# Kernel tuning notes

Measured on AMD Instinct MI355X. Metric: run time of the kernel, lower is better.

## Reference

```python
import jax, jax.numpy as jnp
import numpy as np

VTH = 1.0  # config['v_threshold']
DT = 1.0


def spike_fn(x):
    # forward of ActFun_adp: heaviside(mem - vth)
    return (x > 0).astype(x.dtype)


def setup_inputs() -> dict:
    key = jax.random.key(0)
    k0, k1, k2, k3, k4 = jax.random.split(key, 5)
    B, T, D, H, O = 256, 250, 700, 1024, 20
    input_data = jax.random.normal(k0, (B, T, D), dtype=jnp.float32)
    # dense_1: nn.Linear(700, hidden) default init ~ U(-1/sqrt(D), 1/sqrt(D)); normal/sqrt(D) is an equivalent-scale stand-in
    W1 = jax.random.normal(k1, (H, D), dtype=jnp.float32) / np.sqrt(D).astype(np.float32)
    b1 = jnp.zeros((H,), dtype=jnp.float32)
    tau_m1 = jax.random.uniform(k2, (H,), dtype=jnp.float32, minval=0.0, maxval=4.0)
    # dense_2: xavier_normal_ weight, zero bias
    W2 = jax.random.normal(k3, (O, H), dtype=jnp.float32) * np.sqrt(2.0 / (H + O)).astype(np.float32)
    b2 = jnp.zeros((O,), dtype=jnp.float32)
    tau_m2 = jax.random.uniform(k4, (O,), dtype=jnp.float32, minval=0.0, maxval=4.0)
    return {"input_data": input_data, "W1": W1, "b1": b1, "tau_m1": tau_m1,
            "W2": W2, "b2": b2, "tau_m2": tau_m2}


def reference(input_data, W1, b1, tau_m1, W2, b2, tau_m2):
    B, T, D = input_data.shape
    H = W1.shape[0]
    O = W2.shape[0]
    alpha1 = jax.nn.sigmoid(tau_m1)  # [H]
    alpha2 = jax.nn.sigmoid(tau_m2)  # [O]
    # dense_1 is time-invariant: precompute projections for all timesteps [T,B,H]
    d1_all = (jnp.einsum('btd,hd->bth', input_data, W1) + b1).transpose(1, 0, 2)

    def step(carry, xs):
        mem1, spk1, mem2, acc = carry
        d1_t, i = xs
        # LIF layer 1: soft reset via -vth*spike (mem_update_pra, R_m=1, dt=1)
        mem1 = mem1 * alpha1 + (1.0 - alpha1) * d1_t - VTH * spk1 * DT
        spk1 = spike_fn(mem1 - VTH)
        # readout integrator
        d2 = spk1 @ W2.T + b2
        mem2 = mem2 * alpha2 + (1.0 - alpha2) * d2
        # accumulate softmax for i > 10
        gate = jnp.where(i > 10, jnp.float32(1.0), jnp.float32(0.0))
        acc = acc + gate * jax.nn.softmax(mem2, axis=1)
        return (mem1, spk1, mem2, acc), None

    init = (jnp.zeros((B, H), jnp.float32), jnp.zeros((B, H), jnp.float32),
            jnp.zeros((B, O), jnp.float32), jnp.zeros((B, O), jnp.float32))
    (_, _, _, acc), _ = jax.lax.scan(step, init, (d1_all, jnp.arange(T)))
    return acc
```

## Files before the change

### kernel.cpp

```cpp
#include <hip/hip_runtime.h>
#include <hip/hip_bf16.h>

#define B_  256
#define T_  250
#define D_  700
#define H_  1024
#define O_  20
#define KP  704
#define M_  64000
#define NT  22

typedef __attribute__((ext_vector_type(8))) short bf16x8;
typedef __attribute__((ext_vector_type(4))) float f32x4;

__device__ __forceinline__ void gl_lds16(const void* g, void* l) {
    __builtin_amdgcn_global_load_lds(
        (const __attribute__((address_space(1))) unsigned int*)g,
        (__attribute__((address_space(3))) unsigned int*)l, 16, 0, 0);
}

__global__ void split_convert(const float* __restrict__ src,
                              unsigned short* __restrict__ hi,
                              unsigned short* __restrict__ lo,
                              int M, int Kin, int Kout)
{
    int idx = blockIdx.x * blockDim.x + threadIdx.x;
    int chunks = Kout >> 3;
    int total = M * chunks;
    if (idx >= total) return;
    int m  = idx / chunks;
    int c  = idx - m * chunks;
    int d0 = c << 3;
    float x[8];
    if (d0 + 8 <= Kin) {
        const float4* p = (const float4*)(src + (long)m * Kin + d0);
        float4 v0 = p[0], v1 = p[1];
        x[0] = v0.x; x[1] = v0.y; x[2] = v0.z; x[3] = v0.w;
        x[4] = v1.x; x[5] = v1.y; x[6] = v1.z; x[7] = v1.w;
    } else {
#pragma unroll
        for (int e = 0; e < 8; ++e) {
            int d = d0 + e;
            x[e] = (d < Kin) ? src[(long)m * Kin + d] : 0.0f;
        }
    }
    unsigned short h8[8], l8[8];
#pragma unroll
    for (int e = 0; e < 8; ++e) {
        __hip_bfloat16 h = __float2bfloat16(x[e]);
        float hf = __bfloat162float(h);
        __hip_bfloat16 lv = __float2bfloat16(x[e] - hf);
        h8[e] = *(unsigned short*)&h;
        l8[e] = *(unsigned short*)&lv;
    }
    long ob = (long)m * Kout + d0;
    *(uint4*)(hi + ob) = *(uint4*)h8;
    *(uint4*)(lo + ob) = *(uint4*)l8;
}

#define MF(a,b,c) (c) = __builtin_amdgcn_mfma_f32_16x16x32_bf16((a),(b),(c),0,0,0)

__global__ __launch_bounds__(512, 2) void gemm256(
    const unsigned short* __restrict__ Ahi, const unsigned short* __restrict__ Alo,
    const unsigned short* __restrict__ Bhi, const unsigned short* __restrict__ Blo,
    const float* __restrict__ bias, float* __restrict__ C)
{
    __shared__ __align__(16) unsigned short sAh[2 * 8192];
    __shared__ __align__(16) unsigned short sAl[2 * 8192];
    __shared__ __align__(16) unsigned short sBh[2 * 8192];
    __shared__ __align__(16) unsigned short sBl[2 * 8192];

    const int bid = blockIdx.x;
    const int wg  = (bid & 7) * 125 + (bid >> 3);
    const int mblk = wg >> 2;
    const int nblk = wg & 3;

    const int t    = threadIdx.x;
    const int wave = t >> 6, lane = t & 63;
    const int wr = wave >> 2, wc = wave & 3;

    const int  ch0    = wave * 2;
    const int  rowoff = lane >> 2;
    const int  slotl  = (lane & 3) ^ ((lane >> 3) & 3);
    const long GCH    = 16L * KP;
    const long gArow  = (long)(mblk * 256 + rowoff) * KP + slotl * 8;
    const long gBrow  = (long)(nblk * 256 + rowoff) * KP + slotl * 8;
    const int  ldsl   = ch0 * 512 + lane * 8;

    const int fr   = lane & 15, fq = lane >> 4;
    const int fxor = ((fq ^ ((fr >> 1) & 3)) << 3);
    const int abase = (wr * 128 + fr) * 32 + fxor;
    const int bbase = (wc * 64 + fr) * 32 + fxor;

    f32x4 acc[8][4];
#pragma unroll
    for (int i = 0; i < 8; ++i)
#pragma unroll
        for (int j = 0; j < 4; ++j) acc[i][j] = (f32x4){0.f, 0.f, 0.f, 0.f};

    gl_lds16(Ahi + gArow + ch0 * GCH,       &sAh[ldsl]);
    gl_lds16(Ahi + gArow + (ch0 + 1) * GCH, &sAh[ldsl + 512]);
    gl_lds16(Bhi + gBrow + ch0 * GCH,       &sBh[ldsl]);
    gl_lds16(Bhi + gBrow + (ch0 + 1) * GCH, &sBh[ldsl + 512]);
    gl_lds16(Alo + gArow + ch0 * GCH,       &sAl[ldsl]);
    gl_lds16(Alo + gArow + (ch0 + 1) * GCH, &sAl[ldsl + 512]);
    gl_lds16(Blo + gBrow + ch0 * GCH,       &sBl[ldsl]);
    gl_lds16(Blo + gBrow + (ch0 + 1) * GCH, &sBl[ldsl + 512]);
    asm volatile("s_waitcnt vmcnt(0)" ::: "memory");
    __builtin_amdgcn_s_barrier();

    for (int tt = 0; tt < NT; ++tt) {
        const int  cur = (tt & 1) ? 8192 : 0;
        const int  nxt = 8192 - cur;
        const long ksn = (long)(tt + 1) * 32;
        const bool pf  = (tt + 1 < NT);

        bf16x8 bh[4], bl[4];
#pragma unroll
        for (int p = 0; p < 4; ++p) {
            const int i0 = 2 * p, i1 = 2 * p + 1;
            bf16x8 ah0 = *(const bf16x8*)&sAh[cur + abase + i0 * 512];
            bf16x8 ah1 = *(const bf16x8*)&sAh[cur + abase + i1 * 512];
            bf16x8 al0 = *(const bf16x8*)&sAl[cur + abase + i0 * 512];
            bf16x8 al1 = *(const bf16x8*)&sAl[cur + abase + i1 * 512];
            if (p == 0) {
#pragma unroll
                for (int j = 0; j < 4; ++j) {
                    bh[j] = *(const bf16x8*)&sBh[cur + bbase + j * 512];
                    bl[j] = *(const bf16x8*)&sBl[cur + bbase + j * 512];
                }
            }
            if (p == 0 && pf) {
                gl_lds16(Ahi + gArow + ch0 * GCH + ksn,       &sAh[nxt + ldsl]);
                gl_lds16(Ahi + gArow + (ch0 + 1) * GCH + ksn, &sAh[nxt + ldsl + 512]);
                gl_lds16(Bhi + gBrow + ch0 * GCH + ksn,       &sBh[nxt + ldsl]);
                gl_lds16(Bhi + gBrow + (ch0 + 1) * GCH + ksn, &sBh[nxt + ldsl + 512]);
            }
            if (p == 1 && pf) {
                gl_lds16(Alo + gArow + ch0 * GCH + ksn,       &sAl[nxt + ldsl]);
                gl_lds16(Alo + gArow + (ch0 + 1) * GCH + ksn, &sAl[nxt + ldsl + 512]);
                gl_lds16(Blo + gBrow + ch0 * GCH + ksn,       &sBl[nxt + ldsl]);
                gl_lds16(Blo + gBrow + (ch0 + 1) * GCH + ksn, &sBl[nxt + ldsl + 512]);
            }
            __builtin_amdgcn_s_barrier();
            asm volatile("s_waitcnt lgkmcnt(0)" ::: "memory");
            __builtin_amdgcn_sched_barrier(0);
            __builtin_amdgcn_s_setprio(1);
#pragma unroll
            for (int j = 0; j < 4; ++j) MF(ah0, bh[j], acc[i0][j]);
#pragma unroll
            for (int j = 0; j < 4; ++j) MF(ah1, bh[j], acc[i1][j]);
#pragma unroll
            for (int j = 0; j < 4; ++j) MF(ah0, bl[j], acc[i0][j]);
#pragma unroll
            for (int j = 0; j < 4; ++j) MF(ah1, bl[j], acc[i1][j]);
#pragma unroll
            for (int j = 0; j < 4; ++j) MF(al0, bh[j], acc[i0][j]);
#pragma unroll
            for (int j = 0; j < 4; ++j) MF(al1, bh[j], acc[i1][j]);
            __builtin_amdgcn_s_setprio(0);
            if (p == 3) asm volatile("s_waitcnt vmcnt(0)" ::: "memory");
            __builtin_amdgcn_s_barrier();
        }
    }

    const int r0 = mblk * 256 + wr * 128 + fq * 4;
    const int cc = nblk * 256 + wc * 64 + fr;
#pragma unroll
    for (int j = 0; j < 4; ++j) {
        int col = cc + j * 16;
        float bv = bias[col];
#pragma unroll
        for (int i = 0; i < 8; ++i) {
            int row = r0 + i * 16;
#pragma unroll
            for (int r = 0; r < 4; ++r)
                C[(long)(row + r) * H_ + col] = acc[i][j][r] + bv;
        }
    }
}

__global__ __launch_bounds__(256) void lif_spikes(
    const float* __restrict__ d1,
    const float* __restrict__ tau1,
    unsigned long long* __restrict__ spk)
{
    const int b    = blockIdx.y;
    const int h    = blockIdx.x * 256 + threadIdx.x;
    const int lane = threadIdx.x & 63;
    const int widx = blockIdx.x * 4 + (threadIdx.x >> 6);

    float tv  = tau1[h];
    float a1  = 1.0f / (1.0f + __expf(-tv));
    float om1 = 1.0f - a1;
    float mem = 0.f, sp = 0.f;

    const float* dp = d1 + (long)b * T_ * H_ + h;
    unsigned long long* op = spk + (long)b * T_ * 16 + widx;

    float p0 = dp[0],        p1 = dp[1L * H_], p2 = dp[2L * H_];
    float p3 = dp[3L * H_],  p4 = dp[4L * H_], p5 = dp[5L * H_];

    for (int ts = 0; ts < T_; ++ts) {
        float cur = p0;
        p0 = p1; p1 = p2; p2 = p3; p3 = p4; p4 = p5;
        int nts = ts + 6; nts = (nts < T_) ? nts : (T_ - 1);
        p5 = dp[(long)nts * H_];

        mem = mem * a1 + om1 * cur - sp;
        sp  = (mem > 1.0f) ? 1.0f : 0.0f;
        unsigned long long msk = __ballot(mem > 1.0f);
        if (lane == 0) op[(long)ts * 16] = msk;
    }
}

__global__ __launch_bounds__(256) void readout_dots(
    const unsigned long long* __restrict__ spk,
    const float* __restrict__ W2,
    float* __restrict__ d2t)
{
    const int t = threadIdx.x, wave = t >> 6, lane = t & 63;

    float w2r[5][16];
#pragma unroll
    for (int oo = 0; oo < 5; ++oo)
#pragma unroll
        for (int q = 0; q < 4; ++q)
            *(float4*)&w2r[oo][4 * q] =
                *(const float4*)&W2[(wave * 5 + oo) * H_ + lane * 16 + 4 * q];

    const int rbase = blockIdx.x * 32;
    int b0 = rbase / T_;
    int ts0 = rbase - b0 * T_;

    for (int i = 0; i < 32; i += 2) {
        int r0 = rbase + i, r1 = r0 + 1;
        unsigned long long bw0 = spk[(long)r0 * 16 + (lane >> 2)];
        unsigned long long bw1 = spk[(long)r1 * 16 + (lane >> 2)];
        unsigned int bits0 = (unsigned int)(bw0 >> ((lane & 3) * 16)) & 0xFFFFu;
        unsigned int bits1 = (unsigned int)(bw1 >> ((lane & 3) * 16)) & 0xFFFFu;
        float pa0[5] = {0, 0, 0, 0, 0}, pa1[5] = {0, 0, 0, 0, 0};
#pragma unroll
        for (int j = 0; j < 16; ++j) {
            float f0 = (bits0 >> j) & 1u ? 1.0f : 0.0f;
            float f1 = (bits1 >> j) & 1u ? 1.0f : 0.0f;
#pragma unroll
            for (int oo = 0; oo < 5; ++oo) {
                pa0[oo] = fmaf(f0, w2r[oo][j], pa0[oo]);
                pa1[oo] = fmaf(f1, w2r[oo][j], pa1[oo]);
            }
        }
#pragma unroll
        for (int m = 1; m < 64; m <<= 1)
#pragma unroll
            for (int oo = 0; oo < 5; ++oo) {
                pa0[oo] += __shfl_xor(pa0[oo], m, 64);
                pa1[oo] += __shfl_xor(pa1[oo], m, 64);
            }
        if (lane == 0) {
            int bA = b0, tsA = ts0 + i;
            if (tsA >= T_) { tsA -= T_; bA += 1; }
            int bB = bA, tsB = tsA + 1;
            if (tsB >= T_) { tsB = 0; bB += 1; }
#pragma unroll
            for (int oo = 0; oo < 5; ++oo) {
                d2t[(long)(wave * 5 + oo) * M_ + tsA * 256 + bA] = pa0[oo];
                d2t[(long)(wave * 5 + oo) * M_ + tsB * 256 + bB] = pa1[oo];
            }
        }
    }
}

__global__ __launch_bounds__(64) void mem2_scan(
    const float* __restrict__ d2t,
    const float* __restrict__ tau2, const float* __restrict__ b2,
    float* __restrict__ m2t)
{
    const int o = blockIdx.x;
    const int b = blockIdx.y * 64 + threadIdx.x;
    float tv  = tau2[o];
    float a2  = 1.0f / (1.0f + __expf(-tv));
    float om2 = 1.0f - a2;
    float bv  = b2[o];

    const float* dp = d2t + (long)o * M_ + b;
    float*       mp = m2t + (long)o * M_ + b;
    float mem = 0.f;

    float p0 = dp[0], p1 = dp[256], p2 = dp[512], p3 = dp[768];
    for (int ts = 0; ts < T_; ++ts) {
        float cur = p0; p0 = p1; p1 = p2; p2 = p3;
        int nts = ts + 4; nts = (nts < T_) ? nts : (T_ - 1);
        p3 = dp[(long)nts * 256];
        mem = mem * a2 + om2 * (cur + bv);
        mp[(long)ts * 256] = mem;
    }
}

__global__ __launch_bounds__(256) void softmax_acc(
    const float* __restrict__ m2t,
    float* __restrict__ out)
{
    __shared__ float sp[T_][O_];
    const int b  = blockIdx.x;
    const int ts = threadIdx.x;

    if (ts < T_) {
        if (ts > 10) {
            float m[O_];
#pragma unroll
            for (int o = 0; o < O_; ++o)
                m[o] = m2t[(long)o * M_ + ts * 256 + b];
            float mx = m[0];
#pragma unroll
            for (int o = 1; o < O_; ++o) mx = fmaxf(mx, m[o]);
            float s = 0.f;
#pragma unroll
            for (int o = 0; o < O_; ++o) { m[o] = __expf(m[o] - mx); s += m[o]; }
            float inv = 1.0f / s;
#pragma unroll
            for (int o = 0; o < O_; ++o) sp[ts][o] = m[o] * inv;
        } else {
#pragma unroll
            for (int o = 0; o < O_; ++o) sp[ts][o] = 0.f;
        }
    }
    __syncthreads();
    if (ts < O_) {
        float s = 0.f;
        for (int k = 11; k < T_; ++k) s += sp[k][ts];
        out[b * O_ + ts] = s;
    }
}

extern "C" void kernel_launch(void* const* d_in, const int* in_sizes, int n_in,
                              void* d_out, int out_size, void* d_ws, size_t ws_size,
                              hipStream_t stream)
{
    const float* X    = (const float*)d_in[0];
    const float* W1   = (const float*)d_in[1];
    const float* b1   = (const float*)d_in[2];
    const float* tau1 = (const float*)d_in[3];
    const float* W2   = (const float*)d_in[4];
    const float* b2   = (const float*)d_in[5];
    const float* tau2 = (const float*)d_in[6];
    float* out = (float*)d_out;

    unsigned short* Xhi  = (unsigned short*)d_ws;
    unsigned short* Xlo  = Xhi + (long)M_ * KP;
    unsigned short* W1hi = Xlo + (long)M_ * KP;
    unsigned short* W1lo = W1hi + (long)H_ * KP;
    float* d1 = (float*)(W1lo + (long)H_ * KP);

    unsigned long long* spk = (unsigned long long*)Xhi;
    float* d2t = (float*)Xlo;
    float* m2t = d2t + (long)O_ * M_;

    {
        int chunks = M_ * (KP / 8);
        split_convert<<<(chunks + 255) / 256, 256, 0, stream>>>(X, Xhi, Xlo, M_, D_, KP);
    }
    {
        int chunks = H_ * (KP / 8);
        split_convert<<<(chunks + 255) / 256, 256, 0, stream>>>(W1, W1hi, W1lo, H_, D_, KP);
    }

    gemm256<<<dim3(1000), dim3(512), 0, stream>>>(Xhi, Xlo, W1hi, W1lo, b1, d1);

    {
        dim3 grid(H_ / 256, B_);
        lif_spikes<<<grid, 256, 0, stream>>>(d1, tau1, spk);
    }

    readout_dots<<<M_ / 32, 256, 0, stream>>>(spk, W2, d2t);

    {
        dim3 grid(O_, 4);
        mem2_scan<<<grid, 64, 0, stream>>>(d2t, tau2, b2, m2t);
    }

    softmax_acc<<<B_, 256, 0, stream>>>(m2t, out);
}
```

Baseline: 795.6 us.

## Split GEMM tile loads into staged chunks with partial vmcnt waits and fewer barriers

Reworks the double-buffered K loop of the bf16 split-precision GEMM. Each wave now loads A rows in two groups (rows 0-3 and 4-7 chunks) plus the B chunks, and waits with partial vmcnt counts instead of draining all loads at the end of every K step. This lets compute on the first half of A start while the second half is still arriving. Barriers drop from two per phase to two per K step. The cost is correctness that now depends on a precise vmcnt ordering and on the chunk-to-wave mapping matching the LDS read pattern, which adds risk of races.

```diff
diff --git a/kernel.cpp b/kernel.cpp
--- a/kernel.cpp
+++ b/kernel.cpp
@@ -60,6 +60,28 @@
 
 #define MF(a,b,c) (c) = __builtin_amdgcn_mfma_f32_16x16x32_bf16((a),(b),(c),0,0,0)
 
+__device__ __forceinline__ void phase_mfma(
+    const bf16x8 ah0, const bf16x8 ah1, const bf16x8 al0, const bf16x8 al1,
+    const bf16x8* bh, const bf16x8* bl, f32x4* acc0, f32x4* acc1)
+{
+    asm volatile("s_waitcnt lgkmcnt(0)" ::: "memory");
+    __builtin_amdgcn_sched_barrier(0);
+    __builtin_amdgcn_s_setprio(1);
+#pragma unroll
+    for (int j = 0; j < 4; ++j) MF(ah0, bh[j], acc0[j]);
+#pragma unroll
+    for (int j = 0; j < 4; ++j) MF(ah1, bh[j], acc1[j]);
+#pragma unroll
+    for (int j = 0; j < 4; ++j) MF(ah0, bl[j], acc0[j]);
+#pragma unroll
+    for (int j = 0; j < 4; ++j) MF(ah1, bl[j], acc1[j]);
+#pragma unroll
+    for (int j = 0; j < 4; ++j) MF(al0, bh[j], acc0[j]);
+#pragma unroll
+    for (int j = 0; j < 4; ++j) MF(al1, bh[j], acc1[j]);
+    __builtin_amdgcn_s_setprio(0);
+}
+
 __global__ __launch_bounds__(512, 2) void gemm256(
     const unsigned short* __restrict__ Ahi, const unsigned short* __restrict__ Alo,
     const unsigned short* __restrict__ Bhi, const unsigned short* __restrict__ Blo,
@@ -79,13 +101,35 @@
     const int wave = t >> 6, lane = t & 63;
     const int wr = wave >> 2, wc = wave & 3;
 
-    const int  ch0    = wave * 2;
     const int  rowoff = lane >> 2;
     const int  slotl  = (lane & 3) ^ ((lane >> 3) & 3);
     const long GCH    = 16L * KP;
-    const long gArow  = (long)(mblk * 256 + rowoff) * KP + slotl * 8;
-    const long gBrow  = (long)(nblk * 256 + rowoff) * KP + slotl * 8;
-    const int  ldsl   = ch0 * 512 + lane * 8;
+    const long gA     = (long)(mblk * 256 + rowoff) * KP + slotl * 8;
+    const long gB     = (long)(nblk * 256 + rowoff) * KP + slotl * 8;
+    const int  ldsO   = lane * 8;
+    const int  cB0 = 2 * wave, cB1 = 2 * wave + 1;
+    const int  cA0 = (wave < 4) ? wave : wave + 4;
+    const int  cA1 = cA0 + 4;
+
+    const unsigned short* gBh = Bhi + gB;
+    const unsigned short* gBl = Blo + gB;
+    const unsigned short* gAh = Ahi + gA;
+    const unsigned short* gAl = Alo + gA;
+
+    auto issueB = [&](long ko, int bufo) {
+        gl_lds16(gBh + (long)cB0 * GCH + ko, &sBh[bufo + cB0 * 512 + ldsO]);
+        gl_lds16(gBh + (long)cB1 * GCH + ko, &sBh[bufo + cB1 * 512 + ldsO]);
+        gl_lds16(gBl + (long)cB0 * GCH + ko, &sBl[bufo + cB0 * 512 + ldsO]);
+        gl_lds16(gBl + (long)cB1 * GCH + ko, &sBl[bufo + cB1 * 512 + ldsO]);
+    };
+    auto issueA0 = [&](long ko, int bufo) {
+        gl_lds16(gAh + (long)cA0 * GCH + ko, &sAh[bufo + cA0 * 512 + ldsO]);
+        gl_lds16(gAl + (long)cA0 * GCH + ko, &sAl[bufo + cA0 * 512 + ldsO]);
+    };
+    auto issueA1 = [&](long ko, int bufo) {
+        gl_lds16(gAh + (long)cA1 * GCH + ko, &sAh[bufo + cA1 * 512 + ldsO]);
+        gl_lds16(gAl + (long)cA1 * GCH + ko, &sAl[bufo + cA1 * 512 + ldsO]);
+    };
 
     const int fr   = lane & 15, fq = lane >> 4;
     const int fxor = ((fq ^ ((fr >> 1) & 3)) << 3);
@@ -98,16 +142,7 @@
 #pragma unroll
         for (int j = 0; j < 4; ++j) acc[i][j] = (f32x4){0.f, 0.f, 0.f, 0.f};
 
-    gl_lds16(Ahi + gArow + ch0 * GCH,       &sAh[ldsl]);
-    gl_lds16(Ahi + gArow + (ch0 + 1) * GCH, &sAh[ldsl + 512]);
-    gl_lds16(Bhi + gBrow + ch0 * GCH,       &sBh[ldsl]);
-    gl_lds16(Bhi + gBrow + (ch0 + 1) * GCH, &sBh[ldsl + 512]);
-    gl_lds16(Alo + gArow + ch0 * GCH,       &sAl[ldsl]);
-    gl_lds16(Alo + gArow + (ch0 + 1) * GCH, &sAl[ldsl + 512]);
-    gl_lds16(Blo + gBrow + ch0 * GCH,       &sBl[ldsl]);
-    gl_lds16(Blo + gBrow + (ch0 + 1) * GCH, &sBl[ldsl + 512]);
-    asm volatile("s_waitcnt vmcnt(0)" ::: "memory");
-    __builtin_amdgcn_s_barrier();
+    issueB(0, 0); issueA0(0, 0); issueA1(0, 0);
 
     for (int tt = 0; tt < NT; ++tt) {
         const int  cur = (tt & 1) ? 8192 : 0;
@@ -115,53 +150,43 @@
         const long ksn = (long)(tt + 1) * 32;
         const bool pf  = (tt + 1 < NT);
 
+        asm volatile("s_waitcnt vmcnt(2)" ::: "memory");
+        __builtin_amdgcn_s_barrier();
         bf16x8 bh[4], bl[4];
 #pragma unroll
-        for (int p = 0; p < 4; ++p) {
-            const int i0 = 2 * p, i1 = 2 * p + 1;
-            bf16x8 ah0 = *(const bf16x8*)&sAh[cur + abase + i0 * 512];
-            bf16x8 ah1 = *(const bf16x8*)&sAh[cur + abase + i1 * 512];
-            bf16x8 al0 = *(const bf16x8*)&sAl[cur + abase + i0 * 512];
-            bf16x8 al1 = *(const bf16x8*)&sAl[cur + abase + i1 * 512];
-            if (p == 0) {
-#pragma unroll
-                for (int j = 0; j < 4; ++j) {
-                    bh[j] = *(const bf16x8*)&sBh[cur + bbase + j * 512];
-                    bl[j] = *(const bf16x8*)&sBl[cur + bbase + j * 512];
-                }
-            }
-            if (p == 0 && pf) {
-                gl_lds16(Ahi + gArow + ch0 * GCH + ksn,       &sAh[nxt + ldsl]);
-                gl_lds16(Ahi + gArow + (ch0 + 1) * GCH + ksn, &sAh[nxt + ldsl + 512]);
-                gl_lds16(Bhi + gBrow + ch0 * GCH + ksn,       &sBh[nxt + ldsl]);
-                gl_lds16(Bhi + gBrow + (ch0 + 1) * GCH + ksn, &sBh[nxt + ldsl + 512]);
-            }
-            if (p == 1 && pf) {
-                gl_lds16(Alo + gArow + ch0 * GCH + ksn,       &sAl[nxt + ldsl]);
-                gl_lds16(Alo + gArow + (ch0 + 1) * GCH + ksn, &sAl[nxt + ldsl + 512]);
-                gl_lds16(Blo + gBrow + ch0 * GCH + ksn,       &sBl[nxt + ldsl]);
-                gl_lds16(Blo + gBrow + (ch0 + 1) * GCH + ksn, &sBl[nxt + ldsl + 512]);
-            }
-            __builtin_amdgcn_s_barrier();
-            asm volatile("s_waitcnt lgkmcnt(0)" ::: "memory");
-            __builtin_amdgcn_sched_barrier(0);
-            __builtin_amdgcn_s_setprio(1);
-#pragma unroll
-            for (int j = 0; j < 4; ++j) MF(ah0, bh[j], acc[i0][j]);
-#pragma unroll
-            for (int j = 0; j < 4; ++j) MF(ah1, bh[j], acc[i1][j]);
-#pragma unroll
-            for (int j = 0; j < 4; ++j) MF(ah0, bl[j], acc[i0][j]);
-#pragma unroll
-            for (int j = 0; j < 4; ++j) MF(ah1, bl[j], acc[i1][j]);
-#pragma unroll
-            for (int j = 0; j < 4; ++j) MF(al0, bh[j], acc[i0][j]);
-#pragma unroll
-            for (int j = 0; j < 4; ++j) MF(al1, bh[j], acc[i1][j]);
-            __builtin_amdgcn_s_setprio(0);
-            if (p == 3) asm volatile("s_waitcnt vmcnt(0)" ::: "memory");
-            __builtin_amdgcn_s_barrier();
-        }
+        for (int j = 0; j < 4; ++j) {
+            bh[j] = *(const bf16x8*)&sBh[cur + bbase + j * 512];
+            bl[j] = *(const bf16x8*)&sBl[cur + bbase + j * 512];
+        }
+        bf16x8 a0h = *(const bf16x8*)&sAh[cur + abase + 0 * 512];
+        bf16x8 a1h = *(const bf16x8*)&sAh[cur + abase + 1 * 512];
+        bf16x8 a0l = *(const bf16x8*)&sAl[cur + abase + 0 * 512];
+        bf16x8 a1l = *(const bf16x8*)&sAl[cur + abase + 1 * 512];
+        if (pf) issueB(ksn, nxt);
+        phase_mfma(a0h, a1h, a0l, a1l, bh, bl, acc[0], acc[1]);
+
+        bf16x8 a2h = *(const bf16x8*)&sAh[cur + abase + 2 * 512];
+        bf16x8 a3h = *(const bf16x8*)&sAh[cur + abase + 3 * 512];
+        bf16x8 a2l = *(const bf16x8*)&sAl[cur + abase + 2 * 512];
+        bf16x8 a3l = *(const bf16x8*)&sAl[cur + abase + 3 * 512];
+        if (pf) issueA0(ksn, nxt);
+        phase_mfma(a2h, a3h, a2l, a3l, bh, bl, acc[2], acc[3]);
+
+        if (pf) { asm volatile("s_waitcnt vmcnt(6)" ::: "memory"); }
+        else    { asm volatile("s_waitcnt vmcnt(0)" ::: "memory"); }
+        __builtin_amdgcn_s_barrier();
+        bf16x8 a4h = *(const bf16x8*)&sAh[cur + abase + 4 * 512];
+        bf16x8 a5h = *(const bf16x8*)&sAh[cur + abase + 5 * 512];
+        bf16x8 a4l = *(const bf16x8*)&sAl[cur + abase + 4 * 512];
+        bf16x8 a5l = *(const bf16x8*)&sAl[cur + abase + 5 * 512];
+        if (pf) issueA1(ksn, nxt);
+        phase_mfma(a4h, a5h, a4l, a5l, bh, bl, acc[4], acc[5]);
+
+        bf16x8 a6h = *(const bf16x8*)&sAh[cur + abase + 6 * 512];
+        bf16x8 a7h = *(const bf16x8*)&sAh[cur + abase + 7 * 512];
+        bf16x8 a6l = *(const bf16x8*)&sAl[cur + abase + 6 * 512];
+        bf16x8 a7l = *(const bf16x8*)&sAl[cur + abase + 7 * 512];
+        phase_mfma(a6h, a7h, a6l, a7l, bh, bl, acc[6], acc[7]);
     }
 
     const int r0 = mblk * 256 + wr * 128 + fq * 4;
```

Result: faster. 714.2 us (-10.2%).
